# Kernel tuning notes

Hardware: AMD Instinct MI355X
Metric: run time of the kernel (lower is better)

Reference implementation:

```python
import jax, jax.numpy as jnp
import numpy as np


def setup_inputs() -> dict:
    key = jax.random.key(0)
    k1, k2, k3, k4 = jax.random.split(key, 4)
    H, D, Dh, NH = 4096, 1024, 256, 4  # height, weight1, INNER_FEATURE_A, heads
    x = jax.random.normal(k1, (H, D), dtype=jnp.float32)
    Wq = jax.random.normal(k2, (NH, D, Dh), dtype=jnp.float32)
    lin_w = jax.random.normal(k3, (D, NH * Dh), dtype=jnp.float32)  # torch Linear weight [out, in]
    lin_b = jax.random.normal(k4, (D,), dtype=jnp.float32)
    return {"x": x, "Wq": Wq, "lin_w": lin_w, "lin_b": lin_b}


def reference(x, Wq, lin_w, lin_b):
    # Faithful to source: Q = K = V = x @ Wq1 (original uses Wq1 for all three).
    # mask_flag=False -> multiplicative all-ones mask (identity, elided).
    # qkv: [heads, H, Dh]
    qkv = jnp.einsum('hd,ndk->nhk', x, Wq)
    # scores: [heads, H, H]; softmax over dim=1 of the 2D matrix = last axis here
    scores = jnp.einsum('nqk,npk->nqp', qkv, qkv)
    attn = jax.nn.softmax(scores, axis=-1)
    z = jnp.einsum('nqp,npk->nqk', attn, qkv)  # [heads, H, Dh]
    # concat heads along feature dim -> [H, heads*Dh]
    zc = jnp.transpose(z, (1, 0, 2)).reshape(x.shape[0], -1)
    return zc @ lin_w.T + lin_b
```

## Files before the change

kernel.cpp:

```cpp
#include <hip/hip_runtime.h>
#include <math.h>

#define SEQ 4096
#define DIM 1024
#define DHEAD 256
#define NHEADS 4

typedef __attribute__((ext_vector_type(8))) short bf16x8;
typedef __attribute__((ext_vector_type(4))) float f32x4;
typedef __attribute__((ext_vector_type(4))) short short4v;
typedef __attribute__((ext_vector_type(8))) short short8v;

__device__ __forceinline__ unsigned short f2b(float f) {
    union { float f; unsigned u; } v; v.f = f;
    unsigned r = v.u + 0x7FFFu + ((v.u >> 16) & 1u);
    return (unsigned short)(r >> 16);
}
__device__ __forceinline__ float b2f(unsigned short u) {
    union { unsigned u; float f; } v; v.u = ((unsigned)u) << 16;
    return v.f;
}

__device__ __forceinline__ void gll16(const void* g, void* lds) {
    __builtin_amdgcn_global_load_lds(
        (const __attribute__((address_space(1))) unsigned*)g,
        (__attribute__((address_space(3))) unsigned*)lds, 16, 0, 0);
}

__device__ __forceinline__ f32x4 mfma16(bf16x8 a, bf16x8 b, f32x4 c) {
    return __builtin_amdgcn_mfma_f32_16x16x32_bf16(a, b, c, 0, 0, 0);
}

__global__ __launch_bounds__(256)
void conv_kernel(const float* __restrict__ in, unsigned short* __restrict__ out, int n4) {
    int i = blockIdx.x * 256 + threadIdx.x;
    if (i >= n4) return;
    float4 v = ((const float4*)in)[i];
    short4v o;
    o[0] = (short)f2b(v.x); o[1] = (short)f2b(v.y);
    o[2] = (short)f2b(v.z); o[3] = (short)f2b(v.w);
    *(short4v*)(out + (size_t)i * 4) = o;
}

__global__ __launch_bounds__(256)
void wqt_kernel(const float* __restrict__ Wq, unsigned short* __restrict__ WqT) {
    __shared__ unsigned short T[64][72];
    const int tid = threadIdx.x;
    const int h = blockIdx.z;
    const int d0 = blockIdx.x * 64, c0 = blockIdx.y * 64;
#pragma unroll
    for (int it = 0; it < 4; ++it) {
        int f = tid + 256 * it;
        int row = f >> 4, cg = f & 15;
        float4 v = *(const float4*)&Wq[((size_t)(h * DIM + d0 + row)) * DHEAD + c0 + cg * 4];
        T[row][cg * 4 + 0] = f2b(v.x); T[row][cg * 4 + 1] = f2b(v.y);
        T[row][cg * 4 + 2] = f2b(v.z); T[row][cg * 4 + 3] = f2b(v.w);
    }
    __syncthreads();
#pragma unroll
    for (int it = 0; it < 2; ++it) {
        int f = tid + 256 * it;
        int cl = f >> 3, dg = f & 7;
        short8v o;
#pragma unroll
        for (int e = 0; e < 8; ++e) o[e] = (short)T[dg * 8 + e][cl];
        *(short8v*)&WqT[((size_t)(h * DHEAD + c0 + cl)) * DIM + d0 + dg * 8] = o;
    }
}

__global__ __launch_bounds__(256)
void qkvt_kernel(const unsigned short* __restrict__ qkv, unsigned short* __restrict__ qkvT) {
    __shared__ unsigned short T[64][72];
    const int tid = threadIdx.x;
    const int h = blockIdx.z;
    const int r0 = blockIdx.x * 64, c0 = blockIdx.y * 64;
#pragma unroll
    for (int it = 0; it < 2; ++it) {
        int f = tid + 256 * it;
        int row = f >> 3, cg = f & 7;
        short8v v = *(const short8v*)&qkv[((size_t)h * SEQ + r0 + row) * DHEAD + c0 + cg * 8];
#pragma unroll
        for (int e = 0; e < 8; ++e) T[row][cg * 8 + e] = (unsigned short)v[e];
    }
    __syncthreads();
#pragma unroll
    for (int it = 0; it < 2; ++it) {
        int f = tid + 256 * it;
        int cl = f >> 3, rg = f & 7;
        short8v o;
#pragma unroll
        for (int e = 0; e < 8; ++e) o[e] = (short)T[rg * 8 + e][cl];
        *(short8v*)&qkvT[((size_t)h * DHEAD + c0 + cl) * SEQ + r0 + rg * 8] = o;
    }
}

__global__ __launch_bounds__(256)
void qkv_gemm_kernel(const unsigned short* __restrict__ A,
                     const unsigned short* __restrict__ B,
                     unsigned short* __restrict__ qkv) {
    __shared__ unsigned short As[128 * 64];
    __shared__ unsigned short Bs[128 * 64];
    const int tid = threadIdx.x, w = tid >> 6, l = tid & 63;
    const int g = l >> 4, r16 = l & 15;
    const int m0 = blockIdx.x * 128, n0 = blockIdx.y * 128;
    const int wm = (w >> 1) * 64, wn = (w & 1) * 64;

    f32x4 acc[4][4];
#pragma unroll
    for (int mr = 0; mr < 4; ++mr)
#pragma unroll
        for (int nr = 0; nr < 4; ++nr) acc[mr][nr] = (f32x4){0.f, 0.f, 0.f, 0.f};

    for (int kb = 0; kb < DIM; kb += 64) {
        __syncthreads();
#pragma unroll
        for (int cc = 0; cc < 4; ++cc) {
            int row = w * 32 + cc * 8 + (l >> 3);
            int c = (l & 7) ^ (row & 7);
            gll16(&A[(size_t)(m0 + row) * DIM + kb + c * 8], &As[(size_t)(w * 32 + cc * 8) * 64]);
            gll16(&B[(size_t)(n0 + row) * DIM + kb + c * 8], &Bs[(size_t)(w * 32 + cc * 8) * 64]);
        }
        __syncthreads();
#pragma unroll
        for (int s = 0; s < 2; ++s) {
            bf16x8 af[4], bf[4];
#pragma unroll
            for (int mr = 0; mr < 4; ++mr) {
                int row = wm + mr * 16 + r16;
                int st = (s * 4 + g) ^ (row & 7);
                af[mr] = *(const bf16x8*)&As[row * 64 + st * 8];
            }
#pragma unroll
            for (int nr = 0; nr < 4; ++nr) {
                int row = wn + nr * 16 + r16;
                int st = (s * 4 + g) ^ (row & 7);
                bf[nr] = *(const bf16x8*)&Bs[row * 64 + st * 8];
            }
#pragma unroll
            for (int mr = 0; mr < 4; ++mr)
#pragma unroll
                for (int nr = 0; nr < 4; ++nr)
                    acc[mr][nr] = mfma16(af[mr], bf[nr], acc[mr][nr]);
        }
    }
#pragma unroll
    for (int mr = 0; mr < 4; ++mr)
#pragma unroll
        for (int nr = 0; nr < 4; ++nr) {
            int n = n0 + wn + nr * 16 + r16;
            int h = n >> 8, c = n & 255;
#pragma unroll
            for (int r = 0; r < 4; ++r) {
                int m = m0 + wm + mr * 16 + g * 4 + r;
                qkv[((size_t)h * SEQ + m) * DHEAD + c] = f2b(acc[mr][nr][r]);
            }
        }
}

template<int NSPLIT>
__global__ __launch_bounds__(512, 2)
void attn_kernel(const unsigned short* __restrict__ qkv,
                 const unsigned short* __restrict__ qkvT,
                 unsigned short* __restrict__ p0,
                 unsigned short* __restrict__ p1,
                 unsigned short* __restrict__ p2,
                 unsigned short* __restrict__ p3,
                 float* __restrict__ ml) {
    __shared__ unsigned short Ks[2][64 * 256];
    __shared__ unsigned short Vt[2][256 * 64];
    __shared__ unsigned short Ps[8][16 * 64];

    const int tid = threadIdx.x, w = tid >> 6, l = tid & 63;
    const int g = l >> 4, r16 = l & 15;
    const int bid = blockIdx.x;
    constexpr int CSH = (NSPLIT == 4) ? 4 : 3;
    const int combo = bid & ((1 << CSH) - 1);
    const int h = combo >> ((NSPLIT == 4) ? 2 : 1);
    const int hf = combo & (NSPLIT - 1);
    const int qb = bid >> CSH;
    const unsigned short* __restrict__ qh = qkv + (size_t)h * SEQ * DHEAD;
    const unsigned short* __restrict__ qth = qkvT + (size_t)h * DHEAD * SEQ;
    const int jb0 = hf * (SEQ / NSPLIT);
    const int NT = (SEQ / NSPLIT) / 64;

    bf16x8 qf[2][8];
#pragma unroll
    for (int qs = 0; qs < 2; ++qs) {
        const unsigned short* qrow =
            qh + (size_t)(qb * 256 + w * 32 + qs * 16 + r16) * DHEAD + g * 8;
#pragma unroll
        for (int s = 0; s < 8; ++s) qf[qs][s] = *(const bf16x8*)(qrow + s * 32);
    }

#define STAGEK(buf, jb)                                                             \
    {                                                                               \
        _Pragma("unroll")                                                           \
        for (int cc = 0; cc < 4; ++cc) {                                            \
            int ch = w * 4 + cc;                          \
            int j = ch * 2 + (l >> 5);                                              \
            int cp = l & 31;                                                        \
            int c = (cp & 24) | ((cp & 7) ^ (j & 7));                               \
            gll16(&qh[(size_t)((jb) + j) * DHEAD + c * 8], &Ks[buf][(size_t)ch * 512]); \
        }                                                                           \
    }
#define STAGEV(buf, jb)                                                             \
    {                                                                               \
        _Pragma("unroll")                                                           \
        for (int cc = 0; cc < 4; ++cc) {                                            \
            int ch = w * 4 + cc;                         \
            int d = ch * 8 + (l >> 3);                                              \
            int c = (l & 7) ^ (d & 7);                                              \
            gll16(&qth[(size_t)d * SEQ + (jb) + c * 8], &Vt[buf][(size_t)ch * 512]); \
        }                                                                           \
    }

    STAGEK(0, jb0); STAGEV(0, jb0);
    STAGEK(1, jb0 + 64); STAGEV(1, jb0 + 64);

    f32x4 Oacc[2][16];
#pragma unroll
    for (int qs = 0; qs < 2; ++qs)
#pragma unroll
        for (int i = 0; i < 16; ++i) Oacc[qs][i] = (f32x4){0.f, 0.f, 0.f, 0.f};
    float mrow[2] = {-INFINITY, -INFINITY}, lrow[2] = {0.f, 0.f};

    for (int t = 0; t < NT; ++t) {
        const int cur = t & 1;

        __builtin_amdgcn_sched_barrier(0);
        if (t < NT - 1) { asm volatile("s_waitcnt vmcnt(8)" ::: "memory"); }
        else            { asm volatile("s_waitcnt vmcnt(0)" ::: "memory"); }
        __builtin_amdgcn_s_barrier();
        __builtin_amdgcn_sched_barrier(0);

        const unsigned short* Kb = &Ks[cur][0];
        f32x4 sacc[2][4];
#pragma unroll
        for (int qs = 0; qs < 2; ++qs)
#pragma unroll
            for (int jt = 0; jt < 4; ++jt) sacc[qs][jt] = (f32x4){0.f, 0.f, 0.f, 0.f};
        __builtin_amdgcn_s_setprio(1);
#pragma unroll
        for (int s = 0; s < 8; ++s)
#pragma unroll
            for (int jt = 0; jt < 4; ++jt) {
                int j = jt * 16 + r16;
                int c = s * 4 + g;
                int st = (c & 24) | ((c & 7) ^ (j & 7));
                bf16x8 af = *(const bf16x8*)&Kb[j * 256 + st * 8];
                sacc[0][jt] = mfma16(af, qf[0][s], sacc[0][jt]);
                sacc[1][jt] = mfma16(af, qf[1][s], sacc[1][jt]);
            }
        __builtin_amdgcn_s_setprio(0);

        bf16x8 pa[2][2];
#pragma unroll
        for (int qs = 0; qs < 2; ++qs) {
            float mx = sacc[qs][0][0];
#pragma unroll
            for (int jt = 0; jt < 4; ++jt)
#pragma unroll
                for (int r = 0; r < 4; ++r) mx = fmaxf(mx, sacc[qs][jt][r]);
            mx = fmaxf(mx, __shfl_xor(mx, 16, 64));
            mx = fmaxf(mx, __shfl_xor(mx, 32, 64));

            const bool needr = !__all(mx <= mrow[qs] + 8.f);
            float alpha = 1.f;
            if (needr) {
                float mn = fmaxf(mrow[qs], mx);
                alpha = __expf(mrow[qs] - mn);
                mrow[qs] = mn;
            }

            float rsum = 0.f;
            short4v pf[4];
#pragma unroll
            for (int jt = 0; jt < 4; ++jt)
#pragma unroll
                for (int r = 0; r < 4; ++r) {
                    float p = __expf(sacc[qs][jt][r] - mrow[qs]);
                    rsum += p;
                    pf[jt][r] = (short)f2b(p);
                }
            rsum += __shfl_xor(rsum, 16, 64);
            rsum += __shfl_xor(rsum, 32, 64);
            lrow[qs] = lrow[qs] * alpha + rsum;

#pragma unroll
            for (int jt = 0; jt < 4; ++jt) {
                int st = (2 * jt + (g >> 1)) ^ (r16 & 7);
                *(short4v*)&Ps[w][r16 * 64 + st * 8 + (g & 1) * 4] = pf[jt];
            }

            if (needr) {
                float av[4];
#pragma unroll
                for (int r = 0; r < 4; ++r) av[r] = __shfl(alpha, 4 * g + r, 64);
#pragma unroll
                for (int dt = 0; dt < 16; ++dt)
#pragma unroll
                    for (int r = 0; r < 4; ++r) Oacc[qs][dt][r] *= av[r];
            }

            asm volatile("s_waitcnt lgkmcnt(0)" ::: "memory");
#pragma unroll
            for (int s2 = 0; s2 < 2; ++s2) {
                int st = (4 * s2 + g) ^ (r16 & 7);
                pa[qs][s2] = *(const bf16x8*)&Ps[w][r16 * 64 + st * 8];
            }
            asm volatile("s_waitcnt lgkmcnt(0)" ::: "memory");
        }

        const unsigned short* Vb = &Vt[cur][0];
        __builtin_amdgcn_s_setprio(1);
#pragma unroll
        for (int dt = 0; dt < 16; ++dt) {
            int d = dt * 16 + r16;
#pragma unroll
            for (int s2 = 0; s2 < 2; ++s2) {
                int st = (4 * s2 + g) ^ (d & 7);
                bf16x8 bv = *(const bf16x8*)&Vb[d * 64 + st * 8];
                Oacc[0][dt] = mfma16(pa[0][s2], bv, Oacc[0][dt]);
                Oacc[1][dt] = mfma16(pa[1][s2], bv, Oacc[1][dt]);
            }
        }
        __builtin_amdgcn_s_setprio(0);

        __builtin_amdgcn_sched_barrier(0);
        __builtin_amdgcn_s_barrier();
        __builtin_amdgcn_sched_barrier(0);
        if (t + 2 < NT) {
            const int jb2 = jb0 + (t + 2) * 64;
            STAGEK(cur, jb2); STAGEV(cur, jb2);
        }
        __builtin_amdgcn_sched_barrier(0);
    }
#undef STAGEK
#undef STAGEV

    asm volatile("s_waitcnt vmcnt(0)" ::: "memory");

    unsigned short* po = (hf == 0) ? p0 : (hf == 1) ? p1 : (hf == 2) ? p2 : p3;
#pragma unroll
    for (int qs = 0; qs < 2; ++qs)
#pragma unroll
        for (int dt = 0; dt < 16; ++dt) {
            int d = dt * 16 + r16;
#pragma unroll
            for (int r = 0; r < 4; ++r) {
                int q = qb * 256 + w * 32 + qs * 16 + 4 * g + r;
                po[(size_t)q * (NHEADS * DHEAD) + h * DHEAD + d] = f2b(Oacc[qs][dt][r]);
            }
        }
    if (g == 0) {
#pragma unroll
        for (int qs = 0; qs < 2; ++qs) {
            int q = qb * 256 + w * 32 + qs * 16 + r16;
            float* mlq = ml + ((size_t)(hf * NHEADS + h) * SEQ + q) * 2;
            mlq[0] = mrow[qs]; mlq[1] = lrow[qs];
        }
    }
}

template<int NSPLIT>
__global__ __launch_bounds__(256)
void combine_kernel(const unsigned short* __restrict__ pA,
                    const unsigned short* __restrict__ pB,
                    const unsigned short* __restrict__ pC,
                    const unsigned short* __restrict__ pD,
                    const float* __restrict__ ml,
                    unsigned short* __restrict__ zc) {
    size_t t = (size_t)blockIdx.x * 256 + threadIdx.x;
    size_t f = t * 8;
    int q = (int)(f >> 10);
    int h = (int)((f >> 8) & 3);
    float mm[NSPLIT], lv[NSPLIT];
    float M = -INFINITY;
#pragma unroll
    for (int s = 0; s < NSPLIT; ++s) {
        const float* m = ml + ((size_t)(s * NHEADS + h) * SEQ + q) * 2;
        mm[s] = m[0]; lv[s] = m[1];
        M = fmaxf(M, mm[s]);
    }
    float es[NSPLIT], den = 0.f;
#pragma unroll
    for (int s = 0; s < NSPLIT; ++s) { es[s] = __expf(mm[s] - M); den += es[s] * lv[s]; }
    float inv = 1.f / den;
    const unsigned short* ps[4] = {pA, pB, pC, pD};
    float acc[8] = {0.f, 0.f, 0.f, 0.f, 0.f, 0.f, 0.f, 0.f};
#pragma unroll
    for (int s = 0; s < NSPLIT; ++s) {
        short8v v = *(const short8v*)(ps[s] + f);
#pragma unroll
        for (int e = 0; e < 8; ++e) acc[e] += es[s] * b2f((unsigned short)v[e]);
    }
    short8v o;
#pragma unroll
    for (int e = 0; e < 8; ++e) o[e] = (short)f2b(acc[e] * inv);
    *(short8v*)(zc + f) = o;
}

__global__ __launch_bounds__(256)
void out_gemm_kernel(const unsigned short* __restrict__ A,
                     const unsigned short* __restrict__ B,
                     const float* __restrict__ lb, float* __restrict__ out) {
    __shared__ unsigned short As[128 * 64];
    __shared__ unsigned short Bs[128 * 64];
    const int tid = threadIdx.x, w = tid >> 6, l = tid & 63;
    const int g = l >> 4, r16 = l & 15;
    const int m0 = blockIdx.x * 128, n0 = blockIdx.y * 128;
    const int wm = (w >> 1) * 64, wn = (w & 1) * 64;

    f32x4 acc[4][4];
#pragma unroll
    for (int mr = 0; mr < 4; ++mr)
#pragma unroll
        for (int nr = 0; nr < 4; ++nr) acc[mr][nr] = (f32x4){0.f, 0.f, 0.f, 0.f};

    for (int kb = 0; kb < DIM; kb += 64) {
        __syncthreads();
#pragma unroll
        for (int cc = 0; cc < 4; ++cc) {
            int row = w * 32 + cc * 8 + (l >> 3);
            int c = (l & 7) ^ (row & 7);
            gll16(&A[(size_t)(m0 + row) * DIM + kb + c * 8], &As[(size_t)(w * 32 + cc * 8) * 64]);
            gll16(&B[(size_t)(n0 + row) * DIM + kb + c * 8], &Bs[(size_t)(w * 32 + cc * 8) * 64]);
        }
        __syncthreads();
#pragma unroll
        for (int s = 0; s < 2; ++s) {
            bf16x8 af[4], bf[4];
#pragma unroll
            for (int mr = 0; mr < 4; ++mr) {
                int row = wm + mr * 16 + r16;
                int st = (s * 4 + g) ^ (row & 7);
                af[mr] = *(const bf16x8*)&As[row * 64 + st * 8];
            }
#pragma unroll
            for (int nr = 0; nr < 4; ++nr) {
                int row = wn + nr * 16 + r16;
                int st = (s * 4 + g) ^ (row & 7);
                bf[nr] = *(const bf16x8*)&Bs[row * 64 + st * 8];
            }
#pragma unroll
            for (int mr = 0; mr < 4; ++mr)
#pragma unroll
                for (int nr = 0; nr < 4; ++nr)
                    acc[mr][nr] = mfma16(af[mr], bf[nr], acc[mr][nr]);
        }
    }
#pragma unroll
    for (int mr = 0; mr < 4; ++mr)
#pragma unroll
        for (int nr = 0; nr < 4; ++nr) {
            int n = n0 + wn + nr * 16 + r16;
            float bv = lb[n];
#pragma unroll
            for (int r = 0; r < 4; ++r) {
                int m = m0 + wm + mr * 16 + g * 4 + r;
                out[(size_t)m * DIM + n] = acc[mr][nr][r] + bv;
            }
        }
}

extern "C" void kernel_launch(void* const* d_in, const int* in_sizes, int n_in,
                              void* d_out, int out_size, void* d_ws, size_t ws_size,
                              hipStream_t stream) {
    const float* x  = (const float*)d_in[0];
    const float* Wq = (const float*)d_in[1];
    const float* lw = (const float*)d_in[2];
    const float* lb = (const float*)d_in[3];
    float* out = (float*)d_out;

    char* wsb = (char*)d_ws;
    unsigned short* qkvb = (unsigned short*)(wsb);
    unsigned short* p0   = (unsigned short*)(wsb + ((size_t)8 << 20));
    unsigned short* xb   = (unsigned short*)(wsb + ((size_t)16 << 20));
    unsigned short* p1   = xb;
    unsigned short* WqT  = (unsigned short*)(wsb + ((size_t)24 << 20));
    float*          ml   = (float*)(wsb + ((size_t)24 << 20));
    unsigned short* lwb  = (unsigned short*)(wsb + ((size_t)26 << 20));
    unsigned short* p3   = (unsigned short*)(wsb + ((size_t)28 << 20));
    unsigned short* qkvT = (unsigned short*)d_out;
    unsigned short* p2   = (unsigned short*)d_out + ((size_t)4 << 20);

    conv_kernel<<<4096, 256, 0, stream>>>(x, xb, (SEQ * DIM) / 4);
    conv_kernel<<<1024, 256, 0, stream>>>(lw, lwb, (DIM * DIM) / 4);
    wqt_kernel<<<dim3(16, 4, 4), 256, 0, stream>>>(Wq, WqT);
    qkv_gemm_kernel<<<dim3(SEQ / 128, DIM / 128), 256, 0, stream>>>(xb, WqT, qkvb);
    qkvt_kernel<<<dim3(64, 4, 4), 256, 0, stream>>>(qkvb, qkvT);

    if (ws_size >= ((size_t)36 << 20)) {
        attn_kernel<4><<<256, 512, 0, stream>>>(qkvb, qkvT, p0, p1, p2, p3, ml);
        combine_kernel<4><<<(SEQ * DIM / 8) / 256, 256, 0, stream>>>(p0, p1, p2, p3, ml, p0);
    } else {
        attn_kernel<2><<<128, 512, 0, stream>>>(qkvb, qkvT, p0, p1, p2, p3, ml);
        combine_kernel<2><<<(SEQ * DIM / 8) / 256, 256, 0, stream>>>(p0, p1, p2, p3, ml, p0);
    }
    out_gemm_kernel<<<dim3(SEQ / 128, DIM / 128), 256, 0, stream>>>(p0, lwb, lb, out);
}
```

Before: 170.2 us.

## Shrink attention blocks to 256 threads and drop K/V double buffering

```diff
diff --git a/kernel.cpp b/kernel.cpp
--- a/kernel.cpp
+++ b/kernel.cpp
@@ -158,7 +158,7 @@
 }
 
 template<int NSPLIT>
-__global__ __launch_bounds__(512, 2)
+__global__ __launch_bounds__(256, 2)
 void attn_kernel(const unsigned short* __restrict__ qkv,
                  const unsigned short* __restrict__ qkvT,
                  unsigned short* __restrict__ p0,
@@ -166,9 +166,9 @@
                  unsigned short* __restrict__ p2,
                  unsigned short* __restrict__ p3,
                  float* __restrict__ ml) {
-    __shared__ unsigned short Ks[2][64 * 256];
-    __shared__ unsigned short Vt[2][256 * 64];
-    __shared__ unsigned short Ps[8][16 * 64];
+    __shared__ unsigned short Ks[64 * 256];
+    __shared__ unsigned short Vt[256 * 64];
+    __shared__ unsigned short Ps[4][16 * 64];
 
     const int tid = threadIdx.x, w = tid >> 6, l = tid & 63;
     const int g = l >> 4, r16 = l & 15;
@@ -187,35 +187,32 @@
 #pragma unroll
     for (int qs = 0; qs < 2; ++qs) {
         const unsigned short* qrow =
-            qh + (size_t)(qb * 256 + w * 32 + qs * 16 + r16) * DHEAD + g * 8;
+            qh + (size_t)(qb * 128 + w * 32 + qs * 16 + r16) * DHEAD + g * 8;
 #pragma unroll
         for (int s = 0; s < 8; ++s) qf[qs][s] = *(const bf16x8*)(qrow + s * 32);
     }
 
-#define STAGEK(buf, jb)                                                             \
+#define STAGEK(jb)                                                                  \
     {                                                                               \
         _Pragma("unroll")                                                           \
-        for (int cc = 0; cc < 4; ++cc) {                                            \
-            int ch = w * 4 + cc;                          \
+        for (int cc = 0; cc < 8; ++cc) {                                            \
+            int ch = w * 8 + cc;                          \
             int j = ch * 2 + (l >> 5);                                              \
             int cp = l & 31;                                                        \
             int c = (cp & 24) | ((cp & 7) ^ (j & 7));                               \
-            gll16(&qh[(size_t)((jb) + j) * DHEAD + c * 8], &Ks[buf][(size_t)ch * 512]); \
+            gll16(&qh[(size_t)((jb) + j) * DHEAD + c * 8], &Ks[(size_t)ch * 512]);  \
         }                                                                           \
     }
-#define STAGEV(buf, jb)                                                             \
+#define STAGEV(jb)                                                                  \
     {                                                                               \
         _Pragma("unroll")                                                           \
-        for (int cc = 0; cc < 4; ++cc) {                                            \
-            int ch = w * 4 + cc;                         \
+        for (int cc = 0; cc < 8; ++cc) {                                            \
+            int ch = w * 8 + cc;                         \
             int d = ch * 8 + (l >> 3);                                              \
             int c = (l & 7) ^ (d & 7);                                              \
-            gll16(&qth[(size_t)d * SEQ + (jb) + c * 8], &Vt[buf][(size_t)ch * 512]); \
+            gll16(&qth[(size_t)d * SEQ + (jb) + c * 8], &Vt[(size_t)ch * 512]);     \
         }                                                                           \
     }
-
-    STAGEK(0, jb0); STAGEV(0, jb0);
-    STAGEK(1, jb0 + 64); STAGEV(1, jb0 + 64);
 
     f32x4 Oacc[2][16];
 #pragma unroll
@@ -225,15 +222,13 @@
     float mrow[2] = {-INFINITY, -INFINITY}, lrow[2] = {0.f, 0.f};
 
     for (int t = 0; t < NT; ++t) {
-        const int cur = t & 1;
-
-        __builtin_amdgcn_sched_barrier(0);
-        if (t < NT - 1) { asm volatile("s_waitcnt vmcnt(8)" ::: "memory"); }
-        else            { asm volatile("s_waitcnt vmcnt(0)" ::: "memory"); }
-        __builtin_amdgcn_s_barrier();
-        __builtin_amdgcn_sched_barrier(0);
-
-        const unsigned short* Kb = &Ks[cur][0];
+        const int jb = jb0 + t * 64;
+
+        __syncthreads();
+        STAGEK(jb);
+        STAGEV(jb);
+        __syncthreads();
+
         f32x4 sacc[2][4];
 #pragma unroll
         for (int qs = 0; qs < 2; ++qs)
@@ -247,7 +242,7 @@
                 int j = jt * 16 + r16;
                 int c = s * 4 + g;
                 int st = (c & 24) | ((c & 7) ^ (j & 7));
-                bf16x8 af = *(const bf16x8*)&Kb[j * 256 + st * 8];
+                bf16x8 af = *(const bf16x8*)&Ks[j * 256 + st * 8];
                 sacc[0][jt] = mfma16(af, qf[0][s], sacc[0][jt]);
                 sacc[1][jt] = mfma16(af, qf[1][s], sacc[1][jt]);
             }
@@ -311,7 +306,6 @@
             asm volatile("s_waitcnt lgkmcnt(0)" ::: "memory");
         }
 
-        const unsigned short* Vb = &Vt[cur][0];
         __builtin_amdgcn_s_setprio(1);
 #pragma unroll
         for (int dt = 0; dt < 16; ++dt) {
@@ -319,27 +313,16 @@
 #pragma unroll
             for (int s2 = 0; s2 < 2; ++s2) {
                 int st = (4 * s2 + g) ^ (d & 7);
-                bf16x8 bv = *(const bf16x8*)&Vb[d * 64 + st * 8];
+                bf16x8 bv = *(const bf16x8*)&Vt[d * 64 + st * 8];
                 Oacc[0][dt] = mfma16(pa[0][s2], bv, Oacc[0][dt]);
                 Oacc[1][dt] = mfma16(pa[1][s2], bv, Oacc[1][dt]);
             }
         }
         __builtin_amdgcn_s_setprio(0);
-
-        __builtin_amdgcn_sched_barrier(0);
-        __builtin_amdgcn_s_barrier();
-        __builtin_amdgcn_sched_barrier(0);
-        if (t + 2 < NT) {
-            const int jb2 = jb0 + (t + 2) * 64;
-            STAGEK(cur, jb2); STAGEV(cur, jb2);
-        }
-        __builtin_amdgcn_sched_barrier(0);
     }
 #undef STAGEK
 #undef STAGEV
 
-    asm volatile("s_waitcnt vmcnt(0)" ::: "memory");
-
     unsigned short* po = (hf == 0) ? p0 : (hf == 1) ? p1 : (hf == 2) ? p2 : p3;
 #pragma unroll
     for (int qs = 0; qs < 2; ++qs)
@@ -348,14 +331,14 @@
             int d = dt * 16 + r16;
 #pragma unroll
             for (int r = 0; r < 4; ++r) {
-                int q = qb * 256 + w * 32 + qs * 16 + 4 * g + r;
+                int q = qb * 128 + w * 32 + qs * 16 + 4 * g + r;
                 po[(size_t)q * (NHEADS * DHEAD) + h * DHEAD + d] = f2b(Oacc[qs][dt][r]);
             }
         }
     if (g == 0) {
 #pragma unroll
         for (int qs = 0; qs < 2; ++qs) {
-            int q = qb * 256 + w * 32 + qs * 16 + r16;
+            int q = qb * 128 + w * 32 + qs * 16 + r16;
             float* mlq = ml + ((size_t)(hf * NHEADS + h) * SEQ + q) * 2;
             mlq[0] = mrow[qs]; mlq[1] = lrow[qs];
         }
@@ -491,10 +474,10 @@
     qkvt_kernel<<<dim3(64, 4, 4), 256, 0, stream>>>(qkvb, qkvT);
 
     if (ws_size >= ((size_t)36 << 20)) {
-        attn_kernel<4><<<256, 512, 0, stream>>>(qkvb, qkvT, p0, p1, p2, p3, ml);
+        attn_kernel<4><<<512, 256, 0, stream>>>(qkvb, qkvT, p0, p1, p2, p3, ml);
         combine_kernel<4><<<(SEQ * DIM / 8) / 256, 256, 0, stream>>>(p0, p1, p2, p3, ml, p0);
     } else {
-        attn_kernel<2><<<128, 512, 0, stream>>>(qkvb, qkvT, p0, p1, p2, p3, ml);
+        attn_kernel<2><<<256, 256, 0, stream>>>(qkvb, qkvT, p0, p1, p2, p3, ml);
         combine_kernel<2><<<(SEQ * DIM / 8) / 256, 256, 0, stream>>>(p0, p1, p2, p3, ml, p0);
     }
     out_gemm_kernel<<<dim3(SEQ / 128, DIM / 128), 256, 0, stream>>>(p0, lwb, lb, out);
```

Result: slower. 221.4 us (+30.1%).
